# Kernel optimization log

Hardware: AMD Instinct MI355X
Metric: run time of the kernel (lower is better)

The kernel has to match this reference:

```python
import jax, jax.numpy as jnp
import numpy as np

IN_DIM, DIM, H, L, B, N = 20, 128, 8, 3, 2, 192
DH = DIM // H
EPS = 1e-5


def _conv1d(x, w):
    # x: [b, Cin, n], w: [Cout, Cin, 3], pad=1
    return jax.lax.conv_general_dilated(x, w, (1,), [(1, 1)], dimension_numbers=('NCH', 'OIH', 'NCH'))


def _conv2d(x, w):
    # x: [b, Cin, n, n], w: [Cout, Cin, 3, 3], pad=1
    return jax.lax.conv_general_dilated(x, w, (1, 1), [(1, 1), (1, 1)], dimension_numbers=('NCHW', 'OIHW', 'NCHW'))


def _bn(x, g, b, axes):
    # BatchNorm in training mode (batch statistics, biased variance), channel axis = 1
    m = jnp.mean(x, axes, keepdims=True)
    v = jnp.var(x, axes, keepdims=True)
    sh = [1] * x.ndim
    sh[1] = -1
    return (x - m) / jnp.sqrt(v + EPS) * g.reshape(sh) + b.reshape(sh)


def _ln(x, g, b):
    m = jnp.mean(x, -1, keepdims=True)
    v = jnp.var(x, -1, keepdims=True)
    return (x - m) / jnp.sqrt(v + EPS) * g + b


def _seq2pair(c):
    # c: [b, C, n] -> [b, 2C, n, n]; first C channels constant over j, second C constant over i
    b, C, n = c.shape
    a = jnp.broadcast_to(c[:, :, :, None], (b, C, n, n))
    p = jnp.broadcast_to(c[:, :, None, :], (b, C, n, n))
    return jnp.concatenate([a, p], axis=1)


def _forward(seq, mask, conv1_w, conv2_w, ln_g, ln_b, c1d_w, bn1_g, bn1_b, c2d_w, bn2_g, bn2_b,
             wq_w, wq_b, wk_w, wk_b, wv_w, wv_b, wd_w, wd_b, wl_w, wl_b, fc_w, fc_b):
    b, n, _ = seq.shape
    s = seq.transpose(0, 2, 1)                    # [b, in_dim, n]
    x = _conv1d(s, conv1_w).transpose(0, 2, 1)    # [b, n, dim]
    c = _conv1d(s, conv2_w)                       # [b, dim, n]
    c2 = _seq2pair(c)                             # [b, 2*dim, n, n]
    scale = jnp.sqrt(jnp.asarray(DH, x.dtype))
    m4 = mask[:, None, None, :]                   # [b, 1, 1, n]
    for i in range(L):
        c = jax.nn.relu(_bn(_conv1d(c, c1d_w[i]), bn1_g[i], bn1_b[i], (0, 2)))
        x = _ln(x + c.transpose(0, 2, 1), ln_g[i], ln_b[i])
        c2 = c2 + _seq2pair(c)
        c2 = jax.nn.relu(_bn(_conv2d(c2, c2d_w[i]), bn2_g[i], bn2_b[i], (0, 2, 3)))
        dsym = c2 + c2.transpose(0, 1, 3, 2)      # symmetric pair features [b, 2*dim, n, n]
        gate = jax.nn.sigmoid(jnp.einsum('bcij,hc->bhij', dsym, wd_w[i]) + wd_b[i][None, :, None, None])
        heads = lambda y: y.reshape(b, n, H, DH).transpose(0, 2, 1, 3)
        q = heads(jax.nn.relu(x @ wq_w[i].T + wq_b[i]))
        k = heads(jax.nn.relu(x @ wk_w[i].T + wk_b[i]))
        v = heads(jax.nn.relu(x @ wv_w[i].T + wv_b[i]))
        a = jnp.einsum('bhid,bhjd->bhij', q, k) / scale
        e = jnp.exp(a - jnp.max(a, -1, keepdims=True)) * m4   # hand-rolled masked softmax
        attn = e / (jnp.sum(e, -1, keepdims=True) + 1e-6)
        attn = attn * gate                        # post-softmax multiplicative pair bias
        upd = jnp.einsum('bhij,bhjd->bhid', attn, v).transpose(0, 2, 1, 3).reshape(b, n, DIM)
        x = jax.nn.relu((x + upd) @ wl_w[i].T + wl_b[i])   # dropout = identity (eval)
    return jax.nn.relu(x @ fc_w.T + fc_b)


def setup_inputs():
    key = jax.random.key(0)
    ks = jax.random.split(key, 16)
    rn = lambda k, shape, s=0.05: jax.random.normal(k, shape, jnp.float32) * s
    C2 = 2 * DIM
    return {
        'seq': jax.random.normal(ks[0], (B, N, IN_DIM), jnp.float32),
        'mask': (jax.random.uniform(ks[1], (B, N)) > 0.1).astype(jnp.float32),
        'conv1_w': rn(ks[2], (DIM, IN_DIM, 3)),
        'conv2_w': rn(ks[3], (DIM, IN_DIM, 3)),
        'ln_g': jnp.ones((L, DIM), jnp.float32),
        'ln_b': jnp.zeros((L, DIM), jnp.float32),
        'c1d_w': rn(ks[4], (L, DIM, DIM, 3)),
        'bn1_g': jnp.ones((L, DIM), jnp.float32),
        'bn1_b': jnp.zeros((L, DIM), jnp.float32),
        'c2d_w': rn(ks[5], (L, C2, C2, 3, 3), 0.02),
        'bn2_g': jnp.ones((L, C2), jnp.float32),
        'bn2_b': jnp.zeros((L, C2), jnp.float32),
        'wq_w': rn(ks[6], (L, DIM, DIM)), 'wq_b': jnp.zeros((L, DIM), jnp.float32),
        'wk_w': rn(ks[7], (L, DIM, DIM)), 'wk_b': jnp.zeros((L, DIM), jnp.float32),
        'wv_w': rn(ks[8], (L, DIM, DIM)), 'wv_b': jnp.zeros((L, DIM), jnp.float32),
        'wd_w': rn(ks[9], (L, H, C2)), 'wd_b': jnp.zeros((L, H), jnp.float32),
        'wl_w': rn(ks[10], (L, DIM, DIM)), 'wl_b': jnp.zeros((L, DIM), jnp.float32),
        'fc_w': rn(ks[11], (DIM, DIM)), 'fc_b': jnp.zeros((DIM,), jnp.float32),
    }


def reference(seq, mask, conv1_w, conv2_w, ln_g, ln_b, c1d_w, bn1_g, bn1_b, c2d_w, bn2_g, bn2_b,
              wq_w, wq_b, wk_w, wk_b, wv_w, wv_b, wd_w, wd_b, wl_w, wl_b, fc_w, fc_b):
    return _forward(seq, mask, conv1_w, conv2_w, ln_g, ln_b, c1d_w, bn1_g, bn1_b, c2d_w, bn2_g, bn2_b,
                    wq_w, wq_b, wk_w, wk_b, wv_w, wv_b, wd_w, wd_b, wl_w, wl_b, fc_w, fc_b)
```

## Files before the change

### kernel.cpp

```cpp
#include <hip/hip_runtime.h>
#include <math.h>

#define IN_DIM 20
#define DIM 128
#define HH 8
#define LL 3
#define BB 2
#define NP 192
#define DHH 16
#define C2 256
#define NN (NP*NP)
#define EPS 1e-5f

#define PR 200
#define PC 224

typedef __bf16 bf16x8 __attribute__((ext_vector_type(8)));
typedef float  f32x16 __attribute__((ext_vector_type(16)));

union Pack8 { __bf16 h[8]; uint4 u; };

#define GLOAD16(gp, lp) \
  __builtin_amdgcn_global_load_lds((const __attribute__((address_space(1))) uint4*)(gp), \
                                   (__attribute__((address_space(3))) uint4*)(lp), 16, 0, 0)

__global__ void k_conv_init(const float* __restrict__ seq, const float* __restrict__ w1,
                            const float* __restrict__ w2, float* __restrict__ X,
                            float* __restrict__ Cc) {
  int t = blockIdx.x, b = blockIdx.y, oc = threadIdx.x;
  __shared__ float ss[3][IN_DIM];
  if (threadIdx.x < 3*IN_DIM) {
    int k = threadIdx.x / IN_DIM, ic = threadIdx.x % IN_DIM;
    int tt = t + k - 1;
    ss[k][ic] = (tt >= 0 && tt < NP) ? seq[(b*NP + tt)*IN_DIM + ic] : 0.f;
  }
  __syncthreads();
  float a1 = 0.f, a2 = 0.f;
  #pragma unroll
  for (int ic = 0; ic < IN_DIM; ic++) {
    #pragma unroll
    for (int k = 0; k < 3; k++) {
      float sv = ss[k][ic];
      a1 = fmaf(w1[(oc*IN_DIM + ic)*3 + k], sv, a1);
      a2 = fmaf(w2[(oc*IN_DIM + ic)*3 + k], sv, a2);
    }
  }
  X[(b*NP + t)*DIM + oc] = a1;
  Cc[(b*DIM + oc)*NP + t] = a2;
}

__global__ void k_conv1d_bn_relu(const float* __restrict__ cin, const float* __restrict__ w,
                                 const float* __restrict__ g, const float* __restrict__ bb,
                                 float* __restrict__ cout) {
  int oc = blockIdx.x;
  int t = threadIdx.x;
  float raw[BB];
  for (int b = 0; b < BB; b++) {
    float acc = 0.f;
    for (int ic = 0; ic < DIM; ic++) {
      const float* cr = cin + (b*DIM + ic)*NP;
      const float* wr = w + (oc*DIM + ic)*3;
      float lf = (t > 0)      ? cr[t-1] : 0.f;
      float mf = cr[t];
      float rf = (t < NP-1)   ? cr[t+1] : 0.f;
      acc = fmaf(lf, wr[0], acc);
      acc = fmaf(mf, wr[1], acc);
      acc = fmaf(rf, wr[2], acc);
    }
    raw[b] = acc;
  }
  __shared__ float sb[NP];
  sb[t] = raw[0] + raw[1];
  __syncthreads();
  for (int s = 128; s > 0; s >>= 1) {
    if (t < s && t + s < NP) sb[t] += sb[t + s];
    __syncthreads();
  }
  float mean = sb[0] / (float)(BB*NP);
  __syncthreads();
  sb[t] = raw[0]*raw[0] + raw[1]*raw[1];
  __syncthreads();
  for (int s = 128; s > 0; s >>= 1) {
    if (t < s && t + s < NP) sb[t] += sb[t + s];
    __syncthreads();
  }
  float var = sb[0] / (float)(BB*NP) - mean*mean;
  float rstd = rsqrtf(var + EPS);
  float gg = g[oc], bo = bb[oc];
  for (int b = 0; b < BB; b++)
    cout[(b*DIM + oc)*NP + t] = fmaxf((raw[b] - mean)*rstd*gg + bo, 0.f);
}

__global__ void k_lnqkv(float* __restrict__ X, const float* __restrict__ cc,
                        const float* __restrict__ g, const float* __restrict__ bb,
                        const float* __restrict__ wq, const float* __restrict__ bq,
                        const float* __restrict__ wk, const float* __restrict__ bk,
                        const float* __restrict__ wv, const float* __restrict__ bv,
                        float* __restrict__ Q, float* __restrict__ K, float* __restrict__ V) {
  int t = blockIdx.x, b = blockIdx.y, d = threadIdx.x;
  __shared__ float sb[DIM];
  __shared__ float sy[DIM];
  float v = X[(b*NP + t)*DIM + d] + cc[(b*DIM + d)*NP + t];
  sb[d] = v; __syncthreads();
  for (int s = 64; s > 0; s >>= 1) { if (d < s) sb[d] += sb[d+s]; __syncthreads(); }
  float mean = sb[0] / (float)DIM;
  __syncthreads();
  float dv = v - mean;
  sb[d] = dv*dv; __syncthreads();
  for (int s = 64; s > 0; s >>= 1) { if (d < s) sb[d] += sb[d+s]; __syncthreads(); }
  float var = sb[0] / (float)DIM;
  float rstd = rsqrtf(var + EPS);
  float xn = dv * rstd * g[d] + bb[d];
  X[(b*NP + t)*DIM + d] = xn;
  sy[d] = xn;
  __syncthreads();
  float aq = bq[d], ak = bk[d], av = bv[d];
  for (int e = 0; e < DIM; e++) {
    float xv = sy[e];
    aq = fmaf(wq[d*DIM + e], xv, aq);
    ak = fmaf(wk[d*DIM + e], xv, ak);
    av = fmaf(wv[d*DIM + e], xv, av);
  }
  int h = d >> 4, dh = d & 15;
  size_t o = ((size_t)(b*HH + h)*NP + t)*DHH + dh;
  Q[o] = fmaxf(aq, 0.f); K[o] = fmaxf(ak, 0.f); V[o] = fmaxf(av, 0.f);
}

__global__ void k_wprep(const float* __restrict__ w, __bf16* __restrict__ wtb) {
  int l = blockIdx.x / C2, oc = blockIdx.x % C2;
  int tid = threadIdx.x;
  __shared__ float swt[C2*9];
  const float4* wsrc = (const float4*)(w + ((size_t)(l*C2 + oc))*C2*9);
  for (int idx = tid; idx < 576; idx += 256) ((float4*)swt)[idx] = wsrc[idx];
  __syncthreads();
  for (int v = tid; v < 288; v += 256) {
    int chunk = v / 18, rem = v % 18;
    int kk = rem >> 1, kh = rem & 1;
    Pack8 p;
    #pragma unroll
    for (int e = 0; e < 8; e++)
      p.h[e] = (__bf16)swt[(chunk*16 + kh*8 + e)*9 + kk];
    size_t unit = ((((size_t)(l*16 + chunk)*9 + kk)*2 + kh)*256 + oc);
    ((uint4*)wtb)[unit] = p.u;
  }
}

__global__ void k_make_convin(const float* __restrict__ Cc, const float* __restrict__ CL0,
                              __bf16* __restrict__ inb, float* __restrict__ STATALL) {
  int idx = blockIdx.x*256 + threadIdx.x;
  if (blockIdx.x == 0) {
    for (int z = threadIdx.x; z < 3*2*C2; z += 256) STATALL[z] = 0.f;
  }
  int kh = idx & 1;
  int t = idx >> 1;
  int gcol = t % PC; int t2 = t / PC;
  int grow = t2 % PR; int t3 = t2 / PR;
  int chunk = t3 & 15; int b = t3 >> 4;
  int i = grow - 1, j = gcol - 8;
  Pack8 p;
  if ((unsigned)i < 192u && (unsigned)j < 192u) {
    #pragma unroll
    for (int e = 0; e < 8; e++) {
      int c = chunk*16 + kh*8 + e;
      float v;
      if (c < DIM) v = Cc[(b*DIM + c)*NP + i] + CL0[(b*DIM + c)*NP + i];
      else { int cc = c - DIM; v = Cc[(b*DIM + cc)*NP + j] + CL0[(b*DIM + cc)*NP + j]; }
      p.h[e] = (__bf16)v;
    }
  } else {
    #pragma unroll
    for (int e = 0; e < 8; e++) p.h[e] = (__bf16)0.f;
  }
  ((uint4*)inb)[idx] = p.u;
}

__global__ __launch_bounds__(256, 2)
void k_conv2d_mfma(const __bf16* __restrict__ inb,
                   const __bf16* __restrict__ wtb,
                   __bf16* __restrict__ rawb,
                   float* __restrict__ STAT2) {
  __shared__ __align__(16) uint4 sbuf[2*2176];
  int tid = threadIdx.x;
  int jt = blockIdx.x, it = blockIdx.y, zz = blockIdx.z;
  int b = zz >> 3, oct = zz & 7;
  int i0 = it*8, j0 = jt*64, oc0 = oct*32;
  int lane = tid & 63, wv = tid >> 6;
  int ln31 = lane & 31, khl = lane >> 5;

  const uint4* gW = (const uint4*)wtb;
  const uint4* gI = (const uint4*)inb;

  f32x16 acc[2][2];
  #pragma unroll
  for (int r = 0; r < 2; r++)
    #pragma unroll
    for (int n = 0; n < 2; n++)
      #pragma unroll
      for (int q = 0; q < 16; q++) acc[r][n][q] = 0.f;

  const uint4* gp[9];
  int lofs[9];
  int gstride[9];
  bool gvalid[9];
  #pragma unroll
  for (int t = 0; t < 9; t++) {
    int L = t*4 + wv;
    gvalid[t] = (L < 34);
    if (L < 9) {
      int u = L*64 + lane;
      int kkh = u >> 5;
      int ocl = u & 31;
      gp[t] = gW + (size_t)kkh*256 + oc0 + ocl;
      lofs[t] = u;
      gstride[t] = 4608;
    } else {
      int u = L*64 + lane - 576;
      int r = u / 160;
      int rem = u % 160;
      int kh = rem / 80;
      int c = rem % 80;
      gp[t] = gI + (((size_t)(b*16)*PR) + i0 + r)*PC*2 + (size_t)(j0 + c)*2 + kh;
      lofs[t] = 576 + u;
      gstride[t] = PR*PC*2;
    }
  }

  auto issue = [&](int buf) {
    uint4* lbase = sbuf + buf*2176;
    #pragma unroll
    for (int t = 0; t < 9; t++) {
      if (gvalid[t]) {
        GLOAD16(gp[t], lbase + lofs[t]);
        gp[t] += gstride[t];
      }
    }
  };

  issue(0);

  for (int chunk = 0; chunk < 16; ++chunk) {
    int buf = chunk & 1;
    __syncthreads();
    if (chunk < 15) issue(buf ^ 1);
    const __bf16* Wl = (const __bf16*)(sbuf + buf*2176);
    const __bf16* Il = (const __bf16*)(sbuf + buf*2176 + 576);
    #pragma unroll
    for (int kj = 0; kj < 3; kj++) {
      bf16x8 bfr[4][2];
      #pragma unroll
      for (int rr = 0; rr < 4; rr++) {
        int r = wv*2 + rr;
        #pragma unroll
        for (int ch = 0; ch < 2; ch++) {
          int c = ch*32 + ln31 + kj + 7;
          bfr[rr][ch] = *(const bf16x8*)(Il + ((r*2 + khl)*80 + c)*8);
        }
      }
      #pragma unroll
      for (int ki = 0; ki < 3; ki++) {
        int kk = ki*3 + kj;
        bf16x8 a = *(const bf16x8*)(Wl + ((kk*2 + khl)*32 + ln31)*8);
        #pragma unroll
        for (int row = 0; row < 2; row++)
          #pragma unroll
          for (int ch = 0; ch < 2; ch++)
            acc[row][ch] = __builtin_amdgcn_mfma_f32_32x32x16_bf16(a, bfr[row + ki][ch], acc[row][ch], 0, 0, 0);
      }
    }
  }

  __syncthreads();
  float* trAll = (float*)sbuf;
  float* tr = trAll + wv*(32*33);
  float* sstat = trAll + 4*32*33;
  if (tid < 64) sstat[tid] = 0.f;
  __syncthreads();

  #pragma unroll
  for (int reg = 0; reg < 16; reg++) {
    float v00 = acc[0][0][reg], v01 = acc[0][1][reg];
    float v10 = acc[1][0][reg], v11 = acc[1][1][reg];
    float s = v00 + v01 + v10 + v11;
    float s2 = v00*v00 + v01*v01 + v10*v10 + v11*v11;
    #pragma unroll
    for (int msk = 1; msk <= 16; msk <<= 1) { s += __shfl_xor(s, msk); s2 += __shfl_xor(s2, msk); }
    if (ln31 == 0) {
      int oc_l = (reg & 3) + 8*(reg >> 2) + 4*khl;
      atomicAdd(&sstat[oc_l], s);
      atomicAdd(&sstat[32 + oc_l], s2);
    }
  }

  int Gb = oc0 >> 3;
  uint4* RAWu = (uint4*)rawb;
  #pragma unroll
  for (int row = 0; row < 2; row++) {
    int i = i0 + wv*2 + row;
    #pragma unroll
    for (int ch = 0; ch < 2; ch++) {
      #pragma unroll
      for (int reg = 0; reg < 16; reg++) {
        int r = (reg & 3) + 8*(reg >> 2) + 4*khl;
        tr[r*33 + ln31] = acc[row][ch][reg];
      }
      __builtin_amdgcn_s_waitcnt(0);
      #pragma unroll
      for (int gs = 0; gs < 2; gs++) {
        int g = khl + gs*2;
        Pack8 p;
        #pragma unroll
        for (int e = 0; e < 8; e++) p.h[e] = (__bf16)tr[(g*8 + e)*33 + ln31];
        RAWu[((size_t)(b*32 + Gb + g)*192 + i)*192 + j0 + ch*32 + ln31] = p.u;
      }
      __builtin_amdgcn_s_waitcnt(0);
    }
  }

  __syncthreads();
  if (tid < 32) {
    atomicAdd(&STAT2[oc0 + tid], sstat[tid]);
    atomicAdd(&STAT2[C2 + oc0 + tid], sstat[32 + tid]);
  }
}

template<int WRITE_NEXT>
__global__ void k_bn2_norm_gate(const __bf16* __restrict__ rawb, const float* __restrict__ STAT2,
                                const float* __restrict__ g, const float* __restrict__ bb,
                                const float* __restrict__ wd, const float* __restrict__ CLn,
                                __bf16* __restrict__ inb_next, float* __restrict__ tg) {
  int i = blockIdx.x, b = blockIdx.y, j = threadIdx.x;
  __shared__ float sscale[C2], sshift[C2], swd[HH*C2];
  const float inv = 1.f / (float)(BB*NN);
  for (int c = j; c < C2; c += 192) {
    float mean = STAT2[c] * inv;
    float var  = STAT2[C2 + c] * inv - mean*mean;
    float rstd = rsqrtf(var + EPS);
    float sc = rstd * g[c];
    sscale[c] = sc;
    sshift[c] = bb[c] - mean*sc;
  }
  for (int idx = j; idx < HH*C2; idx += 192) swd[idx] = wd[idx];
  __syncthreads();
  float gacc[HH] = {};
  const uint4* RAWu = (const uint4*)rawb;
  for (int cu = 0; cu < 32; cu++) {
    Pack8 pr; pr.u = RAWu[((size_t)(b*32 + cu)*NP + i)*NP + j];
    Pack8 p;
    #pragma unroll
    for (int e = 0; e < 8; e++) {
      int c = cu*8 + e;
      float v = (float)pr.h[e];
      v = fmaxf(fmaf(v, sscale[c], sshift[c]), 0.f);
      if (WRITE_NEXT) {
        float nv = v + ((c < DIM) ? CLn[(b*DIM + c)*NP + i] : CLn[(b*DIM + c - DIM)*NP + j]);
        p.h[e] = (__bf16)nv;
      }
      #pragma unroll
      for (int h = 0; h < HH; h++) gacc[h] = fmaf(v, swd[h*C2 + c], gacc[h]);
    }
    if (WRITE_NEXT) {
      size_t unit = ((((size_t)(b*16 + (cu>>1))*PR + (i+1))*PC + (j+8))*2 + (cu&1));
      ((uint4*)inb_next)[unit] = p.u;
    }
  }
  for (int h = 0; h < HH; h++)
    tg[((size_t)(b*HH + h)*NP + i)*NP + j] = gacc[h];
}

template<int MODE>
__global__ __launch_bounds__(192)
void k_attnx(const float* __restrict__ Q, const float* __restrict__ K,
             const float* __restrict__ V, const float* __restrict__ tg,
             const float* __restrict__ wdb, const float* __restrict__ mask,
             float* __restrict__ X,
             const float* __restrict__ wl, const float* __restrict__ bl,
             const float* __restrict__ ccn,
             const float* __restrict__ lng, const float* __restrict__ lnb,
             const float* __restrict__ wq, const float* __restrict__ bq,
             const float* __restrict__ wk, const float* __restrict__ bk,
             const float* __restrict__ wv, const float* __restrict__ bv,
             float* __restrict__ Qn, float* __restrict__ Kn, float* __restrict__ Vn,
             const float* __restrict__ fc, const float* __restrict__ fb,
             float* __restrict__ out) {
  int i = blockIdx.x, b = blockIdx.y, j = threadIdx.x;
  int lane = j & 63, wvv = j >> 6;
  __shared__ float sattn[HH][NP];
  __shared__ float supd[DIM];
  __shared__ float sy[DIM];
  __shared__ float sred[3];
  float mk = mask[b*NP + j];

  for (int h = 0; h < HH; h++) {
    size_t bh = (size_t)(b*HH + h);
    const float4* qr = (const float4*)(Q + (bh*NP + i)*DHH);
    const float4* kr = (const float4*)(K + (bh*NP + j)*DHH);
    float a = 0.f;
    #pragma unroll
    for (int q4 = 0; q4 < 4; q4++) {
      float4 qv = qr[q4], kv = kr[q4];
      a = fmaf(qv.x, kv.x, a); a = fmaf(qv.y, kv.y, a);
      a = fmaf(qv.z, kv.z, a); a = fmaf(qv.w, kv.w, a);
    }
    a *= 0.25f;
    float gv = tg[(bh*NP + i)*NP + j] + tg[(bh*NP + j)*NP + i] + wdb[h];
    float gate = 1.f / (1.f + expf(-gv));
    float m = a;
    #pragma unroll
    for (int s = 32; s > 0; s >>= 1) m = fmaxf(m, __shfl_xor(m, s));
    if (lane == 0) sred[wvv] = m;
    __syncthreads();
    float amax = fmaxf(fmaxf(sred[0], sred[1]), sred[2]);
    float e = expf(a - amax) * mk;
    float ss = e;
    #pragma unroll
    for (int s = 32; s > 0; s >>= 1) ss += __shfl_xor(ss, s);
    __syncthreads();
    if (lane == 0) sred[wvv] = ss;
    __syncthreads();
    float denom = sred[0] + sred[1] + sred[2] + 1e-6f;
    sattn[h][j] = (e / denom) * gate;
    __syncthreads();
  }

  if (j < DIM) {
    int h = j >> 4, d = j & 15;
    size_t bh = (size_t)(b*HH + h);
    float acc = 0.f;
    for (int jj = 0; jj < NP; jj++)
      acc = fmaf(sattn[h][jj], V[(bh*NP + jj)*DHH + d], acc);
    supd[h*DHH + d] = acc;
  }
  __syncthreads();

  size_t o = (size_t)(b*NP + i)*DIM;
  if (j < DIM) sy[j] = X[o + j] + supd[j];
  __syncthreads();
  float xr = 0.f;
  if (j < DIM) {
    float acc = bl[j];
    for (int e = 0; e < DIM; e++) acc = fmaf(wl[j*DIM + e], sy[e], acc);
    xr = fmaxf(acc, 0.f);
  }
  __syncthreads();

  if (MODE == 0) {
    float v = 0.f;
    if (j < DIM) v = xr + ccn[(b*DIM + j)*NP + i];
    float s = (j < DIM) ? v : 0.f;
    #pragma unroll
    for (int m = 32; m > 0; m >>= 1) s += __shfl_xor(s, m);
    if (lane == 0 && wvv < 2) sred[wvv] = s;
    __syncthreads();
    float mean = (sred[0] + sred[1]) * (1.f/128.f);
    float dv = v - mean;
    float q = (j < DIM) ? dv*dv : 0.f;
    #pragma unroll
    for (int m = 32; m > 0; m >>= 1) q += __shfl_xor(q, m);
    __syncthreads();
    if (lane == 0 && wvv < 2) sred[wvv] = q;
    __syncthreads();
    float var = (sred[0] + sred[1]) * (1.f/128.f);
    float rstd = rsqrtf(var + EPS);
    if (j < DIM) {
      float xn = dv * rstd * lng[j] + lnb[j];
      X[o + j] = xn;
      sy[j] = xn;
    }
    __syncthreads();
    if (j < DIM) {
      float aq = bq[j], ak = bk[j], av = bv[j];
      for (int e = 0; e < DIM; e++) {
        float xv = sy[e];
        aq = fmaf(wq[j*DIM + e], xv, aq);
        ak = fmaf(wk[j*DIM + e], xv, ak);
        av = fmaf(wv[j*DIM + e], xv, av);
      }
      int h = j >> 4, dh = j & 15;
      size_t oo = ((size_t)(b*HH + h)*NP + i)*DHH + dh;
      Qn[oo] = fmaxf(aq, 0.f); Kn[oo] = fmaxf(ak, 0.f); Vn[oo] = fmaxf(av, 0.f);
    }
  } else {
    if (j < DIM) sy[j] = xr;
    __syncthreads();
    if (j < DIM) {
      float acc = fb[j];
      for (int e = 0; e < DIM; e++) acc = fmaf(fc[j*DIM + e], sy[e], acc);
      out[o + j] = fmaxf(acc, 0.f);
    }
  }
}

extern "C" void kernel_launch(void* const* d_in, const int* in_sizes, int n_in,
                              void* d_out, int out_size, void* d_ws, size_t ws_size,
                              hipStream_t stream) {
  const float* seq     = (const float*)d_in[0];
  const float* mask    = (const float*)d_in[1];
  const float* conv1_w = (const float*)d_in[2];
  const float* conv2_w = (const float*)d_in[3];
  const float* ln_g    = (const float*)d_in[4];
  const float* ln_b    = (const float*)d_in[5];
  const float* c1d_w   = (const float*)d_in[6];
  const float* bn1_g   = (const float*)d_in[7];
  const float* bn1_b   = (const float*)d_in[8];
  const float* c2d_w   = (const float*)d_in[9];
  const float* bn2_g   = (const float*)d_in[10];
  const float* bn2_b   = (const float*)d_in[11];
  const float* wq_w    = (const float*)d_in[12];
  const float* wq_b    = (const float*)d_in[13];
  const float* wk_w    = (const float*)d_in[14];
  const float* wk_b    = (const float*)d_in[15];
  const float* wv_w    = (const float*)d_in[16];
  const float* wv_b    = (const float*)d_in[17];
  const float* wd_w    = (const float*)d_in[18];
  const float* wd_b    = (const float*)d_in[19];
  const float* wl_w    = (const float*)d_in[20];
  const float* wl_b    = (const float*)d_in[21];
  const float* fc_w    = (const float*)d_in[22];
  const float* fc_b    = (const float*)d_in[23];
  float* out = (float*)d_out;

  float* ws = (float*)d_ws;
  float* X    = ws; ws += BB*NP*DIM;
  float* Cc   = ws; ws += BB*DIM*NP;
  float* CL0  = ws; ws += BB*DIM*NP;
  float* CL1  = ws; ws += BB*DIM*NP;
  float* CL2  = ws; ws += BB*DIM*NP;
  float* Q0   = ws; ws += BB*NP*DIM;
  float* K0   = ws; ws += BB*NP*DIM;
  float* V0   = ws; ws += BB*NP*DIM;
  float* Q1   = ws; ws += BB*NP*DIM;
  float* K1   = ws; ws += BB*NP*DIM;
  float* V1   = ws; ws += BB*NP*DIM;
  float* TG0  = ws; ws += (size_t)BB*HH*NN;
  float* TG1  = ws; ws += (size_t)BB*HH*NN;
  float* STATALL = ws; ws += 3*2*C2;
  __bf16* RAW = (__bf16*)ws; ws += (size_t)BB*C2*NN/2;
  __bf16* INB = (__bf16*)ws; ws += (size_t)BB*16*PR*PC*2*16/4;
  __bf16* WTB = (__bf16*)ws; ws += (size_t)LL*C2*C2*9/2;

  k_wprep<<<LL*C2, 256, 0, stream>>>(c2d_w, WTB);
  k_conv_init<<<dim3(NP, BB), DIM, 0, stream>>>(seq, conv1_w, conv2_w, X, Cc);
  k_conv1d_bn_relu<<<DIM, NP, 0, stream>>>(Cc,  c1d_w + 0*(size_t)DIM*DIM*3, bn1_g + 0*DIM, bn1_b + 0*DIM, CL0);
  k_conv1d_bn_relu<<<DIM, NP, 0, stream>>>(CL0, c1d_w + 1*(size_t)DIM*DIM*3, bn1_g + 1*DIM, bn1_b + 1*DIM, CL1);
  k_conv1d_bn_relu<<<DIM, NP, 0, stream>>>(CL1, c1d_w + 2*(size_t)DIM*DIM*3, bn1_g + 2*DIM, bn1_b + 2*DIM, CL2);
  k_make_convin<<<(BB*16*PR*PC*2)/256, 256, 0, stream>>>(Cc, CL0, INB, STATALL);
  k_lnqkv<<<dim3(NP, BB), DIM, 0, stream>>>(X, CL0, ln_g, ln_b,
                                            wq_w, wq_b, wk_w, wk_b, wv_w, wv_b, Q0, K0, V0);

  k_conv2d_mfma<<<dim3(3, 24, 16), 256, 0, stream>>>(INB, WTB + 0*(size_t)16*9*2*256*8, RAW, STATALL + 0*2*C2);
  k_bn2_norm_gate<1><<<dim3(NP, BB), NP, 0, stream>>>(RAW, STATALL + 0*2*C2, bn2_g + 0*C2, bn2_b + 0*C2,
                                                      wd_w + 0*(size_t)HH*C2, CL1, INB, TG0);
  k_attnx<0><<<dim3(NP, BB), NP, 0, stream>>>(Q0, K0, V0, TG0, wd_b + 0*HH, mask, X,
                                              wl_w + 0*(size_t)DIM*DIM, wl_b + 0*DIM,
                                              CL1, ln_g + 1*DIM, ln_b + 1*DIM,
                                              wq_w + 1*(size_t)DIM*DIM, wq_b + 1*DIM,
                                              wk_w + 1*(size_t)DIM*DIM, wk_b + 1*DIM,
                                              wv_w + 1*(size_t)DIM*DIM, wv_b + 1*DIM,
                                              Q1, K1, V1, nullptr, nullptr, nullptr);
  k_conv2d_mfma<<<dim3(3, 24, 16), 256, 0, stream>>>(INB, WTB + 1*(size_t)16*9*2*256*8, RAW, STATALL + 1*2*C2);
  k_bn2_norm_gate<1><<<dim3(NP, BB), NP, 0, stream>>>(RAW, STATALL + 1*2*C2, bn2_g + 1*C2, bn2_b + 1*C2,
                                                      wd_w + 1*(size_t)HH*C2, CL2, INB, TG1);
  k_attnx<0><<<dim3(NP, BB), NP, 0, stream>>>(Q1, K1, V1, TG1, wd_b + 1*HH, mask, X,
                                              wl_w + 1*(size_t)DIM*DIM, wl_b + 1*DIM,
                                              CL2, ln_g + 2*DIM, ln_b + 2*DIM,
                                              wq_w + 2*(size_t)DIM*DIM, wq_b + 2*DIM,
                                              wk_w + 2*(size_t)DIM*DIM, wk_b + 2*DIM,
                                              wv_w + 2*(size_t)DIM*DIM, wv_b + 2*DIM,
                                              Q0, K0, V0, nullptr, nullptr, nullptr);
  k_conv2d_mfma<<<dim3(3, 24, 16), 256, 0, stream>>>(INB, WTB + 2*(size_t)16*9*2*256*8, RAW, STATALL + 2*2*C2);
  k_bn2_norm_gate<0><<<dim3(NP, BB), NP, 0, stream>>>(RAW, STATALL + 2*2*C2, bn2_g + 2*C2, bn2_b + 2*C2,
                                                      wd_w + 2*(size_t)HH*C2, nullptr, nullptr, TG0);
  k_attnx<1><<<dim3(NP, BB), NP, 0, stream>>>(Q0, K0, V0, TG0, wd_b + 2*HH, mask, X,
                                              wl_w + 2*(size_t)DIM*DIM, wl_b + 2*DIM,
                                              nullptr, nullptr, nullptr,
                                              nullptr, nullptr, nullptr, nullptr, nullptr, nullptr,
                                              nullptr, nullptr, nullptr,
                                              fc_w, fc_b, out);
}
```

Before: 682.8 us.

## Transpose dense weights, precompute symmetric gate tiles, batch softmax reductions across heads

Adds a kernel that transposes the q/k/v/l/fc weight matrices once, so the per-row matvecs read weights coalesced across threads instead of with a DIM stride. Adds a tiled gate kernel that symmetrises the pair logits through shared memory and applies the sigmoid, replacing the strided transposed read of tg inside attention. The attention softmax now computes all heads' max and sum reductions together, cutting the many per-head barriers down to a few, and Q is staged in shared memory. This costs extra launches and an extra full gate buffer written and read per layer.

```diff
diff --git a/kernel.cpp b/kernel.cpp
--- a/kernel.cpp
+++ b/kernel.cpp
@@ -91,11 +91,36 @@
     cout[(b*DIM + oc)*NP + t] = fmaxf((raw[b] - mean)*rstd*gg + bo, 0.f);
 }
 
+__global__ void k_wtrans(const float* __restrict__ wq, const float* __restrict__ wk,
+                         const float* __restrict__ wv, const float* __restrict__ wl,
+                         const float* __restrict__ fcw,
+                         float* __restrict__ wqt, float* __restrict__ wkt,
+                         float* __restrict__ wvt, float* __restrict__ wlt,
+                         float* __restrict__ fct) {
+  int m = blockIdx.y;
+  const float* src; float* dst;
+  if (m < 3)       { src = wq + (size_t)m*DIM*DIM;     dst = wqt + (size_t)m*DIM*DIM; }
+  else if (m < 6)  { src = wk + (size_t)(m-3)*DIM*DIM; dst = wkt + (size_t)(m-3)*DIM*DIM; }
+  else if (m < 9)  { src = wv + (size_t)(m-6)*DIM*DIM; dst = wvt + (size_t)(m-6)*DIM*DIM; }
+  else if (m < 12) { src = wl + (size_t)(m-9)*DIM*DIM; dst = wlt + (size_t)(m-9)*DIM*DIM; }
+  else             { src = fcw;                        dst = fct; }
+  int tile = blockIdx.x;
+  int ti = tile >> 2, tj = tile & 3;
+  int r = threadIdx.x >> 3, c4 = threadIdx.x & 7;
+  __shared__ float t[32][33];
+  float4 v = *(const float4*)(src + (ti*32 + r)*DIM + tj*32 + c4*4);
+  t[r][c4*4+0] = v.x; t[r][c4*4+1] = v.y; t[r][c4*4+2] = v.z; t[r][c4*4+3] = v.w;
+  __syncthreads();
+  float4 o;
+  o.x = t[c4*4+0][r]; o.y = t[c4*4+1][r]; o.z = t[c4*4+2][r]; o.w = t[c4*4+3][r];
+  *(float4*)(dst + (tj*32 + r)*DIM + ti*32 + c4*4) = o;
+}
+
 __global__ void k_lnqkv(float* __restrict__ X, const float* __restrict__ cc,
                         const float* __restrict__ g, const float* __restrict__ bb,
-                        const float* __restrict__ wq, const float* __restrict__ bq,
-                        const float* __restrict__ wk, const float* __restrict__ bk,
-                        const float* __restrict__ wv, const float* __restrict__ bv,
+                        const float* __restrict__ wqt, const float* __restrict__ bq,
+                        const float* __restrict__ wkt, const float* __restrict__ bk,
+                        const float* __restrict__ wvt, const float* __restrict__ bv,
                         float* __restrict__ Q, float* __restrict__ K, float* __restrict__ V) {
   int t = blockIdx.x, b = blockIdx.y, d = threadIdx.x;
   __shared__ float sb[DIM];
@@ -117,9 +142,9 @@
   float aq = bq[d], ak = bk[d], av = bv[d];
   for (int e = 0; e < DIM; e++) {
     float xv = sy[e];
-    aq = fmaf(wq[d*DIM + e], xv, aq);
-    ak = fmaf(wk[d*DIM + e], xv, ak);
-    av = fmaf(wv[d*DIM + e], xv, av);
+    aq = fmaf(wqt[e*DIM + d], xv, aq);
+    ak = fmaf(wkt[e*DIM + d], xv, ak);
+    av = fmaf(wvt[e*DIM + d], xv, av);
   }
   int h = d >> 4, dh = d & 15;
   size_t o = ((size_t)(b*HH + h)*NP + t)*DHH + dh;
@@ -367,60 +392,102 @@
     tg[((size_t)(b*HH + h)*NP + i)*NP + j] = gacc[h];
 }
 
+__global__ void k_gate(const float* __restrict__ tg, const float* __restrict__ wdb,
+                       float* __restrict__ gate) {
+  int tile = blockIdx.x;
+  int hb = blockIdx.y;
+  int b = hb >> 3, h = hb & 7;
+  size_t bh = (size_t)(b*HH + h);
+  int ti = tile / 6, tj = tile % 6;
+  int r = threadIdx.x >> 3, c4 = threadIdx.x & 7;
+  __shared__ float tB[32][33];
+  const float* base = tg + bh*NN;
+  float4 vb = *(const float4*)(base + (tj*32 + r)*NP + ti*32 + c4*4);
+  tB[r][c4*4+0] = vb.x; tB[r][c4*4+1] = vb.y; tB[r][c4*4+2] = vb.z; tB[r][c4*4+3] = vb.w;
+  __syncthreads();
+  float4 va = *(const float4*)(base + (ti*32 + r)*NP + tj*32 + c4*4);
+  float bias = wdb[h];
+  float4 o;
+  o.x = 1.f / (1.f + expf(-(va.x + tB[c4*4+0][r] + bias)));
+  o.y = 1.f / (1.f + expf(-(va.y + tB[c4*4+1][r] + bias)));
+  o.z = 1.f / (1.f + expf(-(va.z + tB[c4*4+2][r] + bias)));
+  o.w = 1.f / (1.f + expf(-(va.w + tB[c4*4+3][r] + bias)));
+  *(float4*)(gate + bh*NN + (ti*32 + r)*NP + tj*32 + c4*4) = o;
+}
+
 template<int MODE>
 __global__ __launch_bounds__(192)
 void k_attnx(const float* __restrict__ Q, const float* __restrict__ K,
-             const float* __restrict__ V, const float* __restrict__ tg,
-             const float* __restrict__ wdb, const float* __restrict__ mask,
+             const float* __restrict__ V, const float* __restrict__ gate,
+             const float* __restrict__ mask,
              float* __restrict__ X,
-             const float* __restrict__ wl, const float* __restrict__ bl,
+             const float* __restrict__ wlt, const float* __restrict__ bl,
              const float* __restrict__ ccn,
              const float* __restrict__ lng, const float* __restrict__ lnb,
-             const float* __restrict__ wq, const float* __restrict__ bq,
-             const float* __restrict__ wk, const float* __restrict__ bk,
-             const float* __restrict__ wv, const float* __restrict__ bv,
+             const float* __restrict__ wqt, const float* __restrict__ bq,
+             const float* __restrict__ wkt, const float* __restrict__ bk,
+             const float* __restrict__ wvt, const float* __restrict__ bv,
              float* __restrict__ Qn, float* __restrict__ Kn, float* __restrict__ Vn,
-             const float* __restrict__ fc, const float* __restrict__ fb,
+             const float* __restrict__ fct, const float* __restrict__ fb,
              float* __restrict__ out) {
   int i = blockIdx.x, b = blockIdx.y, j = threadIdx.x;
   int lane = j & 63, wvv = j >> 6;
+  __shared__ float sq[DIM];
   __shared__ float sattn[HH][NP];
   __shared__ float supd[DIM];
   __shared__ float sy[DIM];
+  __shared__ float sredm[HH][3];
+  __shared__ float sreds[HH][3];
   __shared__ float sred[3];
   float mk = mask[b*NP + j];
 
+  if (j < DIM) {
+    int h = j >> 4, d = j & 15;
+    sq[j] = Q[(((size_t)(b*HH + h))*NP + i)*DHH + d];
+  }
+  __syncthreads();
+
+  float a[HH], gt[HH];
+  #pragma unroll
   for (int h = 0; h < HH; h++) {
     size_t bh = (size_t)(b*HH + h);
-    const float4* qr = (const float4*)(Q + (bh*NP + i)*DHH);
     const float4* kr = (const float4*)(K + (bh*NP + j)*DHH);
-    float a = 0.f;
+    const float4* qr = (const float4*)(sq + h*DHH);
+    float acc = 0.f;
     #pragma unroll
     for (int q4 = 0; q4 < 4; q4++) {
       float4 qv = qr[q4], kv = kr[q4];
-      a = fmaf(qv.x, kv.x, a); a = fmaf(qv.y, kv.y, a);
-      a = fmaf(qv.z, kv.z, a); a = fmaf(qv.w, kv.w, a);
-    }
-    a *= 0.25f;
-    float gv = tg[(bh*NP + i)*NP + j] + tg[(bh*NP + j)*NP + i] + wdb[h];
-    float gate = 1.f / (1.f + expf(-gv));
-    float m = a;
+      acc = fmaf(qv.x, kv.x, acc); acc = fmaf(qv.y, kv.y, acc);
+      acc = fmaf(qv.z, kv.z, acc); acc = fmaf(qv.w, kv.w, acc);
+    }
+    a[h] = acc * 0.25f;
+    gt[h] = gate[(bh*NP + i)*NP + j];
+  }
+  #pragma unroll
+  for (int h = 0; h < HH; h++) {
+    float m = a[h];
     #pragma unroll
     for (int s = 32; s > 0; s >>= 1) m = fmaxf(m, __shfl_xor(m, s));
-    if (lane == 0) sred[wvv] = m;
-    __syncthreads();
-    float amax = fmaxf(fmaxf(sred[0], sred[1]), sred[2]);
-    float e = expf(a - amax) * mk;
-    float ss = e;
+    if (lane == 0) sredm[h][wvv] = m;
+  }
+  __syncthreads();
+  float e[HH];
+  #pragma unroll
+  for (int h = 0; h < HH; h++) {
+    float amax = fmaxf(fmaxf(sredm[h][0], sredm[h][1]), sredm[h][2]);
+    e[h] = expf(a[h] - amax) * mk;
+    float ss = e[h];
     #pragma unroll
     for (int s = 32; s > 0; s >>= 1) ss += __shfl_xor(ss, s);
-    __syncthreads();
-    if (lane == 0) sred[wvv] = ss;
-    __syncthreads();
-    float denom = sred[0] + sred[1] + sred[2] + 1e-6f;
-    sattn[h][j] = (e / denom) * gate;
-    __syncthreads();
-  }
+    if (lane == 0) sreds[h][wvv] = ss;
+  }
+  __syncthreads();
+  #pragma unroll
+  for (int h = 0; h < HH; h++) {
+    float denom = sreds[h][0] + sreds[h][1] + sreds[h][2] + 1e-6f;
+    sattn[h][j] = (e[h] / denom) * gt[h];
+  }
+  __syncthreads();
 
   if (j < DIM) {
     int h = j >> 4, d = j & 15;
@@ -438,7 +505,7 @@
   float xr = 0.f;
   if (j < DIM) {
     float acc = bl[j];
-    for (int e = 0; e < DIM; e++) acc = fmaf(wl[j*DIM + e], sy[e], acc);
+    for (int ee = 0; ee < DIM; ee++) acc = fmaf(wlt[ee*DIM + j], sy[ee], acc);
     xr = fmaxf(acc, 0.f);
   }
   __syncthreads();
@@ -469,11 +536,11 @@
     __syncthreads();
     if (j < DIM) {
       float aq = bq[j], ak = bk[j], av = bv[j];
-      for (int e = 0; e < DIM; e++) {
-        float xv = sy[e];
-        aq = fmaf(wq[j*DIM + e], xv, aq);
-        ak = fmaf(wk[j*DIM + e], xv, ak);
-        av = fmaf(wv[j*DIM + e], xv, av);
+      for (int ee = 0; ee < DIM; ee++) {
+        float xv = sy[ee];
+        aq = fmaf(wqt[ee*DIM + j], xv, aq);
+        ak = fmaf(wkt[ee*DIM + j], xv, ak);
+        av = fmaf(wvt[ee*DIM + j], xv, av);
       }
       int h = j >> 4, dh = j & 15;
       size_t oo = ((size_t)(b*HH + h)*NP + i)*DHH + dh;
@@ -484,7 +551,7 @@
     __syncthreads();
     if (j < DIM) {
       float acc = fb[j];
-      for (int e = 0; e < DIM; e++) acc = fmaf(fc[j*DIM + e], sy[e], acc);
+      for (int ee = 0; ee < DIM; ee++) acc = fmaf(fct[ee*DIM + j], sy[ee], acc);
       out[o + j] = fmaxf(acc, 0.f);
     }
   }
@@ -531,13 +598,20 @@
   float* Q1   = ws; ws += BB*NP*DIM;
   float* K1   = ws; ws += BB*NP*DIM;
   float* V1   = ws; ws += BB*NP*DIM;
-  float* TG0  = ws; ws += (size_t)BB*HH*NN;
-  float* TG1  = ws; ws += (size_t)BB*HH*NN;
+  float* TG   = ws; ws += (size_t)BB*HH*NN;
+  float* GATE = ws; ws += (size_t)BB*HH*NN;
+  float* WQT  = ws; ws += (size_t)LL*DIM*DIM;
+  float* WKT  = ws; ws += (size_t)LL*DIM*DIM;
+  float* WVT  = ws; ws += (size_t)LL*DIM*DIM;
+  float* WLT  = ws; ws += (size_t)LL*DIM*DIM;
+  float* FCT  = ws; ws += (size_t)DIM*DIM;
   float* STATALL = ws; ws += 3*2*C2;
   __bf16* RAW = (__bf16*)ws; ws += (size_t)BB*C2*NN/2;
   __bf16* INB = (__bf16*)ws; ws += (size_t)BB*16*PR*PC*2*16/4;
   __bf16* WTB = (__bf16*)ws; ws += (size_t)LL*C2*C2*9/2;
 
+  k_wtrans<<<dim3(16, 13), 256, 0, stream>>>(wq_w, wk_w, wv_w, wl_w, fc_w,
+                                             WQT, WKT, WVT, WLT, FCT);
   k_wprep<<<LL*C2, 256, 0, stream>>>(c2d_w, WTB);
   k_conv_init<<<dim3(NP, BB), DIM, 0, stream>>>(seq, conv1_w, conv2_w, X, Cc);
   k_conv1d_bn_relu<<<DIM, NP, 0, stream>>>(Cc,  c1d_w + 0*(size_t)DIM*DIM*3, bn1_g + 0*DIM, bn1_b + 0*DIM, CL0);
@@ -545,35 +619,38 @@
   k_conv1d_bn_relu<<<DIM, NP, 0, stream>>>(CL1, c1d_w + 2*(size_t)DIM*DIM*3, bn1_g + 2*DIM, bn1_b + 2*DIM, CL2);
   k_make_convin<<<(BB*16*PR*PC*2)/256, 256, 0, stream>>>(Cc, CL0, INB, STATALL);
   k_lnqkv<<<dim3(NP, BB), DIM, 0, stream>>>(X, CL0, ln_g, ln_b,
-                                            wq_w, wq_b, wk_w, wk_b, wv_w, wv_b, Q0, K0, V0);
+                                            WQT, wq_b, WKT, wk_b, WVT, wv_b, Q0, K0, V0);
 
   k_conv2d_mfma<<<dim3(3, 24, 16), 256, 0, stream>>>(INB, WTB + 0*(size_t)16*9*2*256*8, RAW, STATALL + 0*2*C2);
   k_bn2_norm_gate<1><<<dim3(NP, BB), NP, 0, stream>>>(RAW, STATALL + 0*2*C2, bn2_g + 0*C2, bn2_b + 0*C2,
-                                                      wd_w + 0*(size_t)HH*C2, CL1, INB, TG0);
-  k_attnx<0><<<dim3(NP, BB), NP, 0, stream>>>(Q0, K0, V0, TG0, wd_b + 0*HH, mask, X,
-                                              wl_w + 0*(size_t)DIM*DIM, wl_b + 0*DIM,
+                                                      wd_w + 0*(size_t)HH*C2, CL1, INB, TG);
+  k_gate<<<dim3(36, 16), 256, 0, stream>>>(TG, wd_b + 0*HH, GATE);
+  k_attnx<0><<<dim3(NP, BB), NP, 0, stream>>>(Q0, K0, V0, GATE, mask, X,
+                                              WLT + 0*(size_t)DIM*DIM, wl_b + 0*DIM,
                                               CL1, ln_g + 1*DIM, ln_b + 1*DIM,
-                                              wq_w + 1*(size_t)DIM*DIM, wq_b + 1*DIM,
-                                              wk_w + 1*(size_t)DIM*DIM, wk_b + 1*DIM,
-                                              wv_w + 1*(size_t)DIM*DIM, wv_b + 1*DIM,
+                                              WQT + 1*(size_t)DIM*DIM, wq_b + 1*DIM,
+                                              WKT + 1*(size_t)DIM*DIM, wk_b + 1*DIM,
+                                              WVT + 1*(size_t)DIM*DIM, wv_b + 1*DIM,
                                               Q1, K1, V1, nullptr, nullptr, nullptr);
   k_conv2d_mfma<<<dim3(3, 24, 16), 256, 0, stream>>>(INB, WTB + 1*(size_t)16*9*2*256*8, RAW, STATALL + 1*2*C2);
   k_bn2_norm_gate<1><<<dim3(NP, BB), NP, 0, stream>>>(RAW, STATALL + 1*2*C2, bn2_g + 1*C2, bn2_b + 1*C2,
-                                                      wd_w + 1*(size_t)HH*C2, CL2, INB, TG1);
-  k_attnx<0><<<dim3(NP, BB), NP, 0, stream>>>(Q1, K1, V1, TG1, wd_b + 1*HH, mask, X,
-                                              wl_w + 1*(size_t)DIM*DIM, wl_b + 1*DIM,
+                                                      wd_w + 1*(size_t)HH*C2, CL2, INB, TG);
+  k_gate<<<dim3(36, 16), 256, 0, stream>>>(TG, wd_b + 1*HH, GATE);
+  k_attnx<0><<<dim3(NP, BB), NP, 0, stream>>>(Q1, K1, V1, GATE, mask, X,
+                                              WLT + 1*(size_t)DIM*DIM, wl_b + 1*DIM,
                                               CL2, ln_g + 2*DIM, ln_b + 2*DIM,
-                                              wq_w + 2*(size_t)DIM*DIM, wq_b + 2*DIM,
-                                              wk_w + 2*(size_t)DIM*DIM, wk_b + 2*DIM,
-                                              wv_w + 2*(size_t)DIM*DIM, wv_b + 2*DIM,
+                                              WQT + 2*(size_t)DIM*DIM, wq_b + 2*DIM,
+                                              WKT + 2*(size_t)DIM*DIM, wk_b + 2*DIM,
+                                              WVT + 2*(size_t)DIM*DIM, wv_b + 2*DIM,
                                               Q0, K0, V0, nullptr, nullptr, nullptr);
   k_conv2d_mfma<<<dim3(3, 24, 16), 256, 0, stream>>>(INB, WTB + 2*(size_t)16*9*2*256*8, RAW, STATALL + 2*2*C2);
   k_bn2_norm_gate<0><<<dim3(NP, BB), NP, 0, stream>>>(RAW, STATALL + 2*2*C2, bn2_g + 2*C2, bn2_b + 2*C2,
-                                                      wd_w + 2*(size_t)HH*C2, nullptr, nullptr, TG0);
-  k_attnx<1><<<dim3(NP, BB), NP, 0, stream>>>(Q0, K0, V0, TG0, wd_b + 2*HH, mask, X,
-                                              wl_w + 2*(size_t)DIM*DIM, wl_b + 2*DIM,
+                                                      wd_w + 2*(size_t)HH*C2, nullptr, nullptr, TG);
+  k_gate<<<dim3(36, 16), 256, 0, stream>>>(TG, wd_b + 2*HH, GATE);
+  k_attnx<1><<<dim3(NP, BB), NP, 0, stream>>>(Q0, K0, V0, GATE, mask, X,
+                                              WLT + 2*(size_t)DIM*DIM, wl_b + 2*DIM,
                                               nullptr, nullptr, nullptr,
                                               nullptr, nullptr, nullptr, nullptr, nullptr, nullptr,
                                               nullptr, nullptr, nullptr,
-                                              fc_w, fc_b, out);
-}
+                                              FCT, fc_b, out);
+}
```

Result: no change. 680.1 us (-0.4%).
